# Kernel tuning notes

Hardware: AMD Instinct MI355X
Metric: run time of the kernel (lower is better)

## Reference

```python
import jax, jax.numpy as jnp
import numpy as np

NEG = -1e6  # mask fill value used by d2l-style masked_softmax


def setup_inputs() -> dict:
    key = jax.random.key(0)
    kq, kk, kv, kl = jax.random.split(key, 4)
    B, Lq, Lk, D = 8, 2048, 2048, 64
    Q = jax.random.normal(kq, (B, Lq, D), dtype=jnp.float32)
    K = jax.random.normal(kk, (B, Lk, D), dtype=jnp.float32)
    V = jax.random.normal(kv, (B, Lk, D), dtype=jnp.float32)
    valid_len = jax.random.randint(kl, (B,), 1, Lk + 1, dtype=jnp.int64)
    return {"Q": Q, "K": K, "V": V, "valid_len": valid_len}


def reference(Q, K, V, valid_len):
    d = Q.shape[-1]
    scale = 1.0 / jnp.sqrt(jnp.asarray(d, dtype=Q.dtype))
    # scores: [B, Lq, Lk]
    S = jnp.einsum('bqd,bkd->bqk', Q, K) * scale
    Lk = K.shape[1]
    # per-batch key-length mask: position j valid iff j < valid_len[b]
    mask = jnp.arange(Lk)[None, None, :] < valid_len[:, None, None]
    S = jnp.where(mask, S, NEG)
    A = jax.nn.softmax(S, axis=-1)
    return jnp.einsum('bqk,bkd->bqd', A, V)
```

## Files before the change

### kernel.cpp

```cpp
#include <hip/hip_runtime.h>
#include <hip/hip_bf16.h>


constexpr int B_  = 8;
constexpr int L_  = 2048;
constexpr int D_  = 64;
constexpr int LDK = 72;

using bf16x8 = __attribute__((ext_vector_type(8))) __bf16;
using f32x4  = __attribute__((ext_vector_type(4))) float;

__device__ __forceinline__ unsigned short f2bf(float f) {
    unsigned u = __float_as_uint(f);
    u += 0x7FFFu + ((u >> 16) & 1u);
    return (unsigned short)(u >> 16);
}
__device__ __forceinline__ unsigned pack2(float lo, float hi) {
    __hip_bfloat162 h = __float22bfloat162_rn(make_float2(lo, hi));
    return *(unsigned*)&h;
}
__device__ __forceinline__ int sniff_valid(const int* vl, int b) {
    const int p1 = vl[1];
    return (p1 == 0) ? vl[2 * b] : vl[b];
}

__global__ __launch_bounds__(256) void prep(
    const float* __restrict__ Q, const float* __restrict__ K,
    const float* __restrict__ V, unsigned short* __restrict__ Qbf,
    unsigned short* __restrict__ Kbf, unsigned short* __restrict__ Vtb)
{
    const int blk = blockIdx.x, t = threadIdx.x;
    if (blk < 1024) {
        const bool isQ = blk < 512;
        const float* src = isQ ? Q : K;
        unsigned short* dst = isQ ? Qbf : Kbf;
        const float sc = isQ ? 0.125f : 1.0f;
        const size_t base = ((size_t)(isQ ? blk : blk - 512) * 256 + t) * 8;
        float4 a = *(const float4*)(src + base);
        float4 c = *(const float4*)(src + base + 4);
        unsigned us[4] = { pack2(a.x * sc, a.y * sc), pack2(a.z * sc, a.w * sc),
                           pack2(c.x * sc, c.y * sc), pack2(c.z * sc, c.w * sc) };
        *(uint4*)(dst + base) = *(uint4*)us;
    } else {
        __shared__ unsigned short T[64][LDK];
        const int vb = blk - 1024;
        const int b = vb >> 5, lt = vb & 31;
        {
            const int l = t >> 2, d0 = (t & 3) * 16;
            const float* src = V + ((size_t)b * L_ + lt * 64 + l) * D_ + d0;
            #pragma unroll
            for (int p = 0; p < 4; ++p) {
                float4 f = *(const float4*)(src + 4 * p);
                T[d0 + 4*p + 0][l] = f2bf(f.x);
                T[d0 + 4*p + 1][l] = f2bf(f.y);
                T[d0 + 4*p + 2][l] = f2bf(f.z);
                T[d0 + 4*p + 3][l] = f2bf(f.w);
            }
        }
        __syncthreads();
        {
            const int d = t >> 2, k0 = (t & 3) * 16;
            uint4 x0 = *(uint4*)&T[d][k0];
            uint4 x1 = *(uint4*)&T[d][k0 + 8];
            unsigned short* dst = Vtb + ((size_t)b * D_ + d) * L_ + lt * 64 + k0;
            *(uint4*)dst       = x0;
            *(uint4*)(dst + 8) = x1;
        }
    }
}

__global__ __launch_bounds__(256, 4) void attn_fwd(
    const unsigned short* __restrict__ Qbf, const unsigned short* __restrict__ Kbf,
    const unsigned short* __restrict__ Vtb, const int* __restrict__ vl,
    float* __restrict__ O, float* __restrict__ Opart,
    float* __restrict__ lpart, int nsplit, int splitk)
{
    __shared__ __align__(16) unsigned short Ps[4 * 32 * LDK];

    const int tid  = threadIdx.x;
    const int wave = tid >> 6;
    const int lan  = tid & 15;
    const int quad = (tid >> 4) & 3;

    const int wid  = blockIdx.x * 4 + wave;
    const int b    = wid & 7;
    const int rest = wid >> 3;
    const int s    = rest % nsplit;
    const int qg   = rest / nsplit;

    const int valid  = sniff_valid(vl, b);
    const int kstart = s * splitk;
    if (kstart >= valid) return;
    const int kend   = min(kstart + splitk, valid);
    const int ntiles = (kend - kstart + 63) >> 6;

    bf16x8 aq[2][2];
    #pragma unroll
    for (int g = 0; g < 2; ++g) {
        const unsigned short* qp =
            Qbf + ((size_t)b * L_ + qg * 32 + g * 16 + lan) * D_ + quad * 8;
        aq[g][0] = *(const bf16x8*)(qp);
        aq[g][1] = *(const bf16x8*)(qp + 32);
    }

    f32x4 oacc[2][4];
    #pragma unroll
    for (int g = 0; g < 2; ++g)
        #pragma unroll
        for (int c = 0; c < 4; ++c) oacc[g][c] = (f32x4){0.f, 0.f, 0.f, 0.f};
    float lsum[2] = {0.f, 0.f};

    unsigned short* Pw = &Ps[wave * 32 * LDK];
    const unsigned short* Kb = Kbf + (size_t)b * L_ * D_;
    const unsigned short* Vb = Vtb + (size_t)b * D_ * L_;

    for (int t = 0; t < ntiles; ++t) {
        const int kt = kstart + t * 64;

        #pragma unroll
        for (int c = 0; c < 4; ++c) {
            const unsigned short* kp = Kb + (size_t)(kt + c * 16 + lan) * D_ + quad * 8;
            bf16x8 ak0 = *(const bf16x8*)(kp);
            bf16x8 ak1 = *(const bf16x8*)(kp + 32);
            f32x4 z0 = (f32x4){0.f, 0.f, 0.f, 0.f};
            f32x4 z1 = (f32x4){0.f, 0.f, 0.f, 0.f};
            z0 = __builtin_amdgcn_mfma_f32_16x16x32_bf16(ak0, aq[0][0], z0, 0, 0, 0);
            z1 = __builtin_amdgcn_mfma_f32_16x16x32_bf16(ak0, aq[1][0], z1, 0, 0, 0);
            z0 = __builtin_amdgcn_mfma_f32_16x16x32_bf16(ak1, aq[0][1], z0, 0, 0, 0);
            z1 = __builtin_amdgcn_mfma_f32_16x16x32_bf16(ak1, aq[1][1], z1, 0, 0, 0);

            const int kbase = kt + c * 16 + quad * 4;
            float p0[4], p1[4];
            #pragma unroll
            for (int r = 0; r < 4; ++r) {
                const bool ok = (kbase + r) < valid;
                p0[r] = ok ? __expf(z0[r]) : 0.f;
                p1[r] = ok ? __expf(z1[r]) : 0.f;
                lsum[0] += p0[r];
                lsum[1] += p1[r];
            }
            *(uint2*)&Pw[lan * LDK + c * 16 + quad * 4] =
                make_uint2(pack2(p0[0], p0[1]), pack2(p0[2], p0[3]));
            *(uint2*)&Pw[(16 + lan) * LDK + c * 16 + quad * 4] =
                make_uint2(pack2(p1[0], p1[1]), pack2(p1[2], p1[3]));
        }

        bf16x8 ap[2][2];
        #pragma unroll
        for (int g = 0; g < 2; ++g) {
            ap[g][0] = *(const bf16x8*)&Pw[(g*16 + lan) * LDK + quad * 8];
            ap[g][1] = *(const bf16x8*)&Pw[(g*16 + lan) * LDK + 32 + quad * 8];
        }
        #pragma unroll
        for (int c = 0; c < 4; ++c) {
            const unsigned short* vp = Vb + (size_t)(c * 16 + lan) * L_ + kt + quad * 8;
            bf16x8 bv0 = *(const bf16x8*)(vp);
            bf16x8 bv1 = *(const bf16x8*)(vp + 32);
            #pragma unroll
            for (int g = 0; g < 2; ++g) {
                oacc[g][c] = __builtin_amdgcn_mfma_f32_16x16x32_bf16(ap[g][0], bv0, oacc[g][c], 0, 0, 0);
                oacc[g][c] = __builtin_amdgcn_mfma_f32_16x16x32_bf16(ap[g][1], bv1, oacc[g][c], 0, 0, 0);
            }
        }
    }

    #pragma unroll
    for (int g = 0; g < 2; ++g) {
        lsum[g] += __shfl_xor(lsum[g], 16);
        lsum[g] += __shfl_xor(lsum[g], 32);
    }

    const int rowbase = qg * 32;
    if (nsplit == 1) {
        #pragma unroll
        for (int g = 0; g < 2; ++g) {
            float inv[4];
            #pragma unroll
            for (int r = 0; r < 4; ++r)
                inv[r] = 1.0f / __shfl(lsum[g], quad * 4 + r);
            float* Og = O + ((size_t)b * L_ + rowbase + g * 16) * D_;
            #pragma unroll
            for (int c = 0; c < 4; ++c)
                #pragma unroll
                for (int r = 0; r < 4; ++r)
                    Og[(size_t)(quad * 4 + r) * D_ + c * 16 + lan] = oacc[g][c][r] * inv[r];
        }
    } else {
        #pragma unroll
        for (int g = 0; g < 2; ++g) {
            float* Og = Opart + ((size_t)s * B_ * L_ + (size_t)b * L_ + rowbase + g * 16) * D_;
            #pragma unroll
            for (int c = 0; c < 4; ++c)
                #pragma unroll
                for (int r = 0; r < 4; ++r)
                    Og[(size_t)(quad * 4 + r) * D_ + c * 16 + lan] = oacc[g][c][r];
            if (quad == 0)
                lpart[(size_t)s * B_ * L_ + (size_t)b * L_ + rowbase + g * 16 + lan] = lsum[g];
        }
    }
}

__global__ __launch_bounds__(256) void attn_combine(
    const float* __restrict__ Opart, const float* __restrict__ lpart,
    const int* __restrict__ vl, float* __restrict__ O,
    int nsplit, int splitk)
{
    const int idx = blockIdx.x * 256 + threadIdx.x;
    const int row = idx >> 4;
    const int b   = row >> 11;
    const int off = (idx & 15) * 4;
    const int valid = sniff_valid(vl, b);
    const int ns = min(nsplit, (valid + splitk - 1) / splitk);

    float Lsum = 0.f;
    float4 acc = make_float4(0.f, 0.f, 0.f, 0.f);
    for (int s = 0; s < ns; ++s) {
        Lsum += lpart[s * (B_ * L_) + row];
        float4 o4 = *(const float4*)&Opart[(size_t)s * (B_ * L_ * D_) + (size_t)row * D_ + off];
        acc.x += o4.x; acc.y += o4.y; acc.z += o4.z; acc.w += o4.w;
    }
    const float inv = 1.0f / Lsum;
    acc.x *= inv; acc.y *= inv; acc.z *= inv; acc.w *= inv;
    *(float4*)&O[(size_t)row * D_ + off] = acc;
}

extern "C" void kernel_launch(void* const* d_in, const int* in_sizes, int n_in,
                              void* d_out, int out_size, void* d_ws, size_t ws_size,
                              hipStream_t stream) {
    const float* Q  = (const float*)d_in[0];
    const float* K  = (const float*)d_in[1];
    const float* V  = (const float*)d_in[2];
    const int*   vl = (const int*)d_in[3];
    float* O = (float*)d_out;

    const size_t nElem  = (size_t)B_ * L_ * D_;
    const size_t prepB  = 3 * nElem * sizeof(unsigned short);
    auto need = [&](int n) {
        return prepB + (size_t)n * (nElem + B_ * L_) * sizeof(float);
    };
    int nsplit = 1;
    if      (ws_size >= need(8)) nsplit = 8;
    else if (ws_size >= need(4)) nsplit = 4;
    else if (ws_size >= need(2)) nsplit = 2;
    const int splitk = L_ / nsplit;

    unsigned short* Qbf = (unsigned short*)d_ws;
    unsigned short* Kbf = Qbf + nElem;
    unsigned short* Vtb = Kbf + nElem;
    float* Opart = (float*)(Vtb + nElem);
    float* lpart = Opart + (size_t)nsplit * nElem;

    prep<<<dim3(1280), 256, 0, stream>>>(Q, K, V, Qbf, Kbf, Vtb);
    attn_fwd<<<dim3(128 * nsplit), 256, 0, stream>>>(
        Qbf, Kbf, Vtb, vl, O, Opart, lpart, nsplit, splitk);
    if (nsplit > 1)
        attn_combine<<<dim3((B_ * L_ * D_ / 4) / 256), 256, 0, stream>>>(
            Opart, lpart, vl, O, nsplit, splitk);
}
```

Measured before the change: 106.4 us.

## Share K/V tiles in LDS across four waves with register prefetch

Each block now covers 128 query rows, with its four waves sharing K and V tiles staged in LDS, where before each wave loaded K/V from global memory on its own. The next tile is prefetched into registers while the current one is computed. Block-to-work mapping is rearranged for the split-8 case, and softmax uses exp2 with log2e folded into the Q scaling. This cuts global and L2 traffic for K/V, at the cost of two barriers per tile and more LDS per block, which may lower occupancy.

```diff
diff --git a/kernel.cpp b/kernel.cpp
--- a/kernel.cpp
+++ b/kernel.cpp
@@ -5,7 +5,10 @@
 constexpr int B_  = 8;
 constexpr int L_  = 2048;
 constexpr int D_  = 64;
+constexpr int BQ  = 128;
 constexpr int LDK = 72;
+constexpr int NQ  = L_ / BQ;
+#define LOG2E 1.44269504088896f
 
 using bf16x8 = __attribute__((ext_vector_type(8))) __bf16;
 using f32x4  = __attribute__((ext_vector_type(4))) float;
@@ -34,7 +37,7 @@
         const bool isQ = blk < 512;
         const float* src = isQ ? Q : K;
         unsigned short* dst = isQ ? Qbf : Kbf;
-        const float sc = isQ ? 0.125f : 1.0f;
+        const float sc = isQ ? 0.125f * LOG2E : 1.0f;
         const size_t base = ((size_t)(isQ ? blk : blk - 512) * 256 + t) * 8;
         float4 a = *(const float4*)(src + base);
         float4 c = *(const float4*)(src + base + 4);
@@ -75,18 +78,27 @@
     float* __restrict__ O, float* __restrict__ Opart,
     float* __restrict__ lpart, int nsplit, int splitk)
 {
+    __shared__ __align__(16) unsigned short Ks[64 * LDK];
+    __shared__ __align__(16) unsigned short Vt[64 * LDK];
     __shared__ __align__(16) unsigned short Ps[4 * 32 * LDK];
 
+    const int id = blockIdx.x;
+    int b, qt, s;
+    if (nsplit == 8) {
+        const int x = id & 7, j = id >> 3;
+        b  = j & 7;
+        qt = j >> 3;
+        s  = (x - b) & 7;
+    } else {
+        b = id & 7;
+        const int r = id >> 3;
+        qt = r & (NQ - 1);
+        s  = r >> 4;
+    }
     const int tid  = threadIdx.x;
     const int wave = tid >> 6;
     const int lan  = tid & 15;
     const int quad = (tid >> 4) & 3;
-
-    const int wid  = blockIdx.x * 4 + wave;
-    const int b    = wid & 7;
-    const int rest = wid >> 3;
-    const int s    = rest % nsplit;
-    const int qg   = rest / nsplit;
 
     const int valid  = sniff_valid(vl, b);
     const int kstart = s * splitk;
@@ -94,11 +106,26 @@
     const int kend   = min(kstart + splitk, valid);
     const int ntiles = (kend - kstart + 63) >> 6;
 
+    const unsigned short* Kb = Kbf + (size_t)b * L_ * D_;
+    const unsigned short* Vb = Vtb + (size_t)b * D_ * L_;
+
+    const int srow = tid >> 2, sseg = (tid & 3) * 16;
+
+    uint4 kpre[2], vpre[2];
+    {
+        const unsigned short* kp = Kb + (size_t)(kstart + srow) * D_ + sseg;
+        kpre[0] = *(const uint4*)(kp);
+        kpre[1] = *(const uint4*)(kp + 8);
+        const unsigned short* vp = Vb + (size_t)srow * L_ + kstart + sseg;
+        vpre[0] = *(const uint4*)(vp);
+        vpre[1] = *(const uint4*)(vp + 8);
+    }
+
     bf16x8 aq[2][2];
     #pragma unroll
     for (int g = 0; g < 2; ++g) {
         const unsigned short* qp =
-            Qbf + ((size_t)b * L_ + qg * 32 + g * 16 + lan) * D_ + quad * 8;
+            Qbf + ((size_t)b * L_ + qt * BQ + wave * 32 + g * 16 + lan) * D_ + quad * 8;
         aq[g][0] = *(const bf16x8*)(qp);
         aq[g][1] = *(const bf16x8*)(qp + 32);
     }
@@ -111,17 +138,30 @@
     float lsum[2] = {0.f, 0.f};
 
     unsigned short* Pw = &Ps[wave * 32 * LDK];
-    const unsigned short* Kb = Kbf + (size_t)b * L_ * D_;
-    const unsigned short* Vb = Vtb + (size_t)b * D_ * L_;
 
     for (int t = 0; t < ntiles; ++t) {
         const int kt = kstart + t * 64;
+        __syncthreads();
+
+        *(uint4*)&Ks[srow * LDK + sseg]     = kpre[0];
+        *(uint4*)&Ks[srow * LDK + sseg + 8] = kpre[1];
+        *(uint4*)&Vt[srow * LDK + sseg]     = vpre[0];
+        *(uint4*)&Vt[srow * LDK + sseg + 8] = vpre[1];
+        __syncthreads();
+
+        if (t + 1 < ntiles) {
+            const unsigned short* kp = Kb + (size_t)(kt + 64 + srow) * D_ + sseg;
+            kpre[0] = *(const uint4*)(kp);
+            kpre[1] = *(const uint4*)(kp + 8);
+            const unsigned short* vp = Vb + (size_t)srow * L_ + kt + 64 + sseg;
+            vpre[0] = *(const uint4*)(vp);
+            vpre[1] = *(const uint4*)(vp + 8);
+        }
 
         #pragma unroll
         for (int c = 0; c < 4; ++c) {
-            const unsigned short* kp = Kb + (size_t)(kt + c * 16 + lan) * D_ + quad * 8;
-            bf16x8 ak0 = *(const bf16x8*)(kp);
-            bf16x8 ak1 = *(const bf16x8*)(kp + 32);
+            bf16x8 ak0 = *(const bf16x8*)&Ks[(c*16 + lan) * LDK + quad * 8];
+            bf16x8 ak1 = *(const bf16x8*)&Ks[(c*16 + lan) * LDK + 32 + quad * 8];
             f32x4 z0 = (f32x4){0.f, 0.f, 0.f, 0.f};
             f32x4 z1 = (f32x4){0.f, 0.f, 0.f, 0.f};
             z0 = __builtin_amdgcn_mfma_f32_16x16x32_bf16(ak0, aq[0][0], z0, 0, 0, 0);
@@ -134,8 +174,8 @@
             #pragma unroll
             for (int r = 0; r < 4; ++r) {
                 const bool ok = (kbase + r) < valid;
-                p0[r] = ok ? __expf(z0[r]) : 0.f;
-                p1[r] = ok ? __expf(z1[r]) : 0.f;
+                p0[r] = ok ? exp2f(z0[r]) : 0.f;
+                p1[r] = ok ? exp2f(z1[r]) : 0.f;
                 lsum[0] += p0[r];
                 lsum[1] += p1[r];
             }
@@ -153,9 +193,8 @@
         }
         #pragma unroll
         for (int c = 0; c < 4; ++c) {
-            const unsigned short* vp = Vb + (size_t)(c * 16 + lan) * L_ + kt + quad * 8;
-            bf16x8 bv0 = *(const bf16x8*)(vp);
-            bf16x8 bv1 = *(const bf16x8*)(vp + 32);
+            bf16x8 bv0 = *(const bf16x8*)&Vt[(c*16 + lan) * LDK + quad * 8];
+            bf16x8 bv1 = *(const bf16x8*)&Vt[(c*16 + lan) * LDK + 32 + quad * 8];
             #pragma unroll
             for (int g = 0; g < 2; ++g) {
                 oacc[g][c] = __builtin_amdgcn_mfma_f32_16x16x32_bf16(ap[g][0], bv0, oacc[g][c], 0, 0, 0);
@@ -170,7 +209,7 @@
         lsum[g] += __shfl_xor(lsum[g], 32);
     }
 
-    const int rowbase = qg * 32;
+    const int rowbase = qt * BQ + wave * 32;
     if (nsplit == 1) {
         #pragma unroll
         for (int g = 0; g < 2; ++g) {
@@ -233,8 +272,8 @@
     const int*   vl = (const int*)d_in[3];
     float* O = (float*)d_out;
 
-    const size_t nElem  = (size_t)B_ * L_ * D_;
-    const size_t prepB  = 3 * nElem * sizeof(unsigned short);
+    const size_t nElem = (size_t)B_ * L_ * D_;
+    const size_t prepB = 3 * nElem * sizeof(unsigned short);
     auto need = [&](int n) {
         return prepB + (size_t)n * (nElem + B_ * L_) * sizeof(float);
     };
@@ -251,7 +290,7 @@
     float* lpart = Opart + (size_t)nsplit * nElem;
 
     prep<<<dim3(1280), 256, 0, stream>>>(Q, K, V, Qbf, Kbf, Vtb);
-    attn_fwd<<<dim3(128 * nsplit), 256, 0, stream>>>(
+    attn_fwd<<<dim3(nsplit * B_ * NQ), 256, 0, stream>>>(
         Qbf, Kbf, Vtb, vl, O, Opart, lpart, nsplit, splitk);
     if (nsplit > 1)
         attn_combine<<<dim3((B_ * L_ * D_ / 4) / 256), 256, 0, stream>>>(
```

After: 99.20 us. 6.8% less time.
